# Optimization experiments

Measured on AMD Instinct MI355X. Metric: run time of the kernel, lower is better.

The kernel has to match this reference:

```python
import jax, jax.numpy as jnp
import numpy as np

HIDDEN = 4096
INTER = 11008
BATCH, SEQ = 2, 2048


def setup_inputs() -> dict:
    key = jax.random.key(0)
    ks = jax.random.split(key, 7)
    s_h = 1.0 / np.sqrt(HIDDEN)   # nn.Linear default init bound fan_in=HIDDEN
    s_i = 1.0 / np.sqrt(INTER)    # fan_in=INTER for down_proj
    return {
        "hidden_states": jax.random.normal(ks[0], (BATCH, SEQ, HIDDEN), dtype=jnp.float32),
        "w_gate": jax.random.uniform(ks[1], (INTER, HIDDEN), jnp.float32, -s_h, s_h),
        "b_gate": jax.random.uniform(ks[2], (INTER,), jnp.float32, -s_h, s_h),
        "w_up": jax.random.uniform(ks[3], (INTER, HIDDEN), jnp.float32, -s_h, s_h),
        "b_up": jax.random.uniform(ks[4], (INTER,), jnp.float32, -s_h, s_h),
        "w_down": jax.random.uniform(ks[5], (HIDDEN, INTER), jnp.float32, -s_i, s_i),
        "b_down": jax.random.uniform(ks[6], (HIDDEN,), jnp.float32, -s_i, s_i),
    }


def reference(hidden_states, w_gate, b_gate, w_up, b_up, w_down, b_down):
    # SwiGLU MLP: down( silu(gate(x)) * up(x) )
    gate = jax.nn.silu(jnp.einsum("bsh,ih->bsi", hidden_states, w_gate) + b_gate)
    up = jnp.einsum("bsh,ih->bsi", hidden_states, w_up) + b_up
    return jnp.einsum("bsi,hi->bsh", gate * up, w_down) + b_down
```

## Files before the change

kernel.cpp:

```cpp
#include <hip/hip_runtime.h>
#include <hip/hip_bf16.h>


#define M_TOK 4096
#define HID   4096
#define INT_  11008
#define NGU   1376
#define NCVT  160

typedef __attribute__((ext_vector_type(8))) short bf16x8;
typedef __attribute__((ext_vector_type(4))) float f32x4;

__device__ __forceinline__ unsigned short f2bf(float f) {
    union { float f; unsigned int u; } a; a.f = f;
    unsigned int u = a.u;
    u += 0x7fff + ((u >> 16) & 1);
    return (unsigned short)(u >> 16);
}

__global__ void cvt3(const float* __restrict__ x,  unsigned short* __restrict__ xb,
                     const float* __restrict__ wg, unsigned short* __restrict__ s1,
                     const float* __restrict__ wu, unsigned short* __restrict__ s2,
                     int n4x, int n4w) {
    const int total = n4x + 2 * n4w;
    const int stride = gridDim.x * blockDim.x;
    for (int i = blockIdx.x * blockDim.x + threadIdx.x; i < total; i += stride) {
        const float* src; unsigned short* dst; int j;
        if (i < n4x)            { j = i;             src = x;  dst = xb; }
        else if (i < n4x + n4w) { j = i - n4x;       src = wg; dst = s1; }
        else                    { j = i - n4x - n4w; src = wu; dst = s2; }
        float4 v = ((const float4*)src)[j];
        ushort4 o;
        o.x = f2bf(v.x); o.y = f2bf(v.y); o.z = f2bf(v.z); o.w = f2bf(v.w);
        ((ushort4*)dst)[j] = o;
    }
}

__global__ void cvt_f32_bf16(const float* __restrict__ in, unsigned short* __restrict__ out, int n4) {
    int stride = gridDim.x * blockDim.x;
    for (int i = blockIdx.x * blockDim.x + threadIdx.x; i < n4; i += stride) {
        float4 v = ((const float4*)in)[i];
        ushort4 o;
        o.x = f2bf(v.x); o.y = f2bf(v.y); o.z = f2bf(v.z); o.w = f2bf(v.w);
        ((ushort4*)out)[i] = o;
    }
}

#define GLL(gsrc, ldst) \
    __builtin_amdgcn_global_load_lds( \
        (__attribute__((address_space(1))) void*)(gsrc), \
        (__attribute__((address_space(3))) void*)(ldst), 16, 0, 0)

#define VMC(n) asm volatile("s_waitcnt vmcnt(" #n ")" ::: "memory")
#define BARR __builtin_amdgcn_s_barrier()
#define PIN  __builtin_amdgcn_sched_barrier(0)

__global__ __launch_bounds__(512, 2)
void gemm_gu(const unsigned short* __restrict__ A,
             const unsigned short* __restrict__ Wg,
             const unsigned short* __restrict__ Wu,
             const float* __restrict__ bg,
             const float* __restrict__ bu,
             unsigned short* __restrict__ T,
             const float* __restrict__ wdSrc,
             unsigned short* __restrict__ wdDst,
             int M, int NI, int K) {
    __shared__ unsigned short lds[2 * 32768];

    const int tid  = threadIdx.x;

    if (blockIdx.x >= NGU) {
        const int c = blockIdx.x - NGU;
        const int n4w = (INT_ * HID) / 4;
        const float4* src = (const float4*)wdSrc;
        ushort4* dst = (ushort4*)wdDst;
        for (int u = c * 512 + tid; u < n4w; u += NCVT * 512) {
            float4 v = src[u];
            ushort4 o;
            o.x = f2bf(v.x); o.y = f2bf(v.y); o.z = f2bf(v.z); o.w = f2bf(v.w);
            dst[u] = o;
        }
        return;
    }

    const int lane = tid & 63;
    const int w    = tid >> 6;
    const int wm   = w >> 2;
    const int wn   = w & 3;

    const int ntn = NI >> 7;
    const int chunk = NGU >> 3;
    const int sw = (blockIdx.x & 7) * chunk + (blockIdx.x >> 3);
    const int bm = sw / ntn, bn = sw % ntn;

    const unsigned short* Ag  = A  + (size_t)(bm * 256) * K;
    const unsigned short* Bgg = Wg + (size_t)(bn * 128) * K;
    const unsigned short* Bug = Wu + (size_t)(bn * 128) * K;

    int offA[2][2], offBW[2];
#pragma unroll
    for (int i = 0; i < 2; ++i) {
        int sig = i * 512 + tid;
        int r   = sig >> 3;
        int s   = (sig & 7) ^ (r & 7);
#pragma unroll
        for (int h = 0; h < 2; ++h) {
            int grow = ((r >> 6) * 2 + h) * 64 + (r & 63);
            offA[h][i] = grow * K + s * 8;
        }
        offBW[i] = r * K + s * 8;
    }

    const int rl = lane & 15;
    const int kg = lane >> 4;
    const int x  = rl & 7;
    const int aRow  = (wm * 64 + rl) * 64;
    const int bGoff = 16384 + (wn * 32 + rl) * 64;
    const int bUoff = 24576 + (wn * 32 + rl) * 64;
    int slt[2];
#pragma unroll
    for (int ks = 0; ks < 2; ++ks) slt[ks] = ((ks * 4 + kg) ^ x) * 8;

    f32x4 accg[2][8], accu[2][8];
#pragma unroll
    for (int q = 0; q < 2; ++q)
#pragma unroll
        for (int f = 0; f < 8; ++f) {
            accg[q][f] = (f32x4){0.f, 0.f, 0.f, 0.f};
            accu[q][f] = (f32x4){0.f, 0.f, 0.f, 0.f};
        }

    const int NT = K >> 6;

#define STAGE_A(H, DST, SRC) \
    GLL((SRC) + offA[H][0], (DST) + (H) * 8192 + tid * 8); \
    GLL((SRC) + offA[H][1], (DST) + (H) * 8192 + 4096 + tid * 8)
#define STAGE_W(BASE, DST, SRC) \
    GLL((SRC) + offBW[0], (DST) + (BASE) + tid * 8); \
    GLL((SRC) + offBW[1], (DST) + (BASE) + 4096 + tid * 8)

#define RD_A(BUF, QM, DST) \
    { _Pragma("unroll") for (int ks = 0; ks < 2; ++ks) \
      _Pragma("unroll") for (int fm = 0; fm < 4; ++fm) \
        DST[ks * 4 + fm] = *(const bf16x8*)((BUF) + (QM) * 8192 + aRow + fm * 1024 + slt[ks]); }
#define RD_W(BUF, ROFF, DST) \
    { _Pragma("unroll") for (int ks = 0; ks < 2; ++ks) \
      _Pragma("unroll") for (int fn = 0; fn < 2; ++fn) \
        DST[ks * 2 + fn] = *(const bf16x8*)((BUF) + (ROFF) + fn * 1024 + slt[ks]); }
#define Q16(ACC, QM, AF, BF) \
    { _Pragma("unroll") for (int ks = 0; ks < 2; ++ks) \
      _Pragma("unroll") for (int fm = 0; fm < 4; ++fm) \
      _Pragma("unroll") for (int fn = 0; fn < 2; ++fn) \
        ACC[QM][fm * 2 + fn] = __builtin_amdgcn_mfma_f32_16x16x32_bf16( \
            AF[ks * 4 + fm], BF[ks * 2 + fn], ACC[QM][fm * 2 + fn], 0, 0, 0); }

    bf16x8 A0f[8], A1f[8], Bgf[4], Buf_[4];

    STAGE_A(0, lds, Ag);
    STAGE_W(16384, lds, Bgg);
    STAGE_W(24576, lds, Bug);
    STAGE_A(1, lds, Ag);
    VMC(2);
    BARR; PIN;

    for (int t = 0; t < NT; ++t) {
        const unsigned short* bc = lds + (t & 1) * 32768;
        unsigned short* sb = lds + ((t + 1) & 1) * 32768;
        const int ts = (t + 1 < NT) ? (t + 1) : (NT - 1);
        const unsigned short* sA = Ag + (size_t)ts * 64;
        const unsigned short* sG = Bgg + (size_t)ts * 64;
        const unsigned short* sU = Bug + (size_t)ts * 64;

        RD_A(bc, 0, A0f);
        RD_W(bc, bGoff, Bgf);
        STAGE_A(0, sb, sA);
        Q16(accg, 0, A0f, Bgf);
        RD_W(bc, bUoff, Buf_);
        STAGE_W(16384, sb, sG);
        Q16(accu, 0, A0f, Buf_);
        STAGE_W(24576, sb, sU);
        VMC(6);
        BARR; PIN;

        RD_A(bc, 1, A1f);
        STAGE_A(1, sb, sA);
        Q16(accg, 1, A1f, Bgf);
        Q16(accu, 1, A1f, Buf_);
        VMC(2);
        BARR; PIN;
    }
#undef RD_A
#undef RD_W
#undef Q16
#undef STAGE_A
#undef STAGE_W

    const int rbase = bm * 256 + wm * 128 + (lane >> 4) * 4;
    const int cbase = bn * 128 + wn * 32 + (lane & 15);
#pragma unroll
    for (int qm = 0; qm < 2; ++qm)
#pragma unroll
        for (int fn = 0; fn < 2; ++fn) {
            const int col = cbase + fn * 16;
            const float bgv = bg[col];
            const float buv = bu[col];
#pragma unroll
            for (int fm = 0; fm < 4; ++fm) {
                const int rb = rbase + qm * 64 + fm * 16;
#pragma unroll
                for (int j = 0; j < 4; ++j) {
                    float g = accg[qm][fm * 2 + fn][j] + bgv;
                    float u = accu[qm][fm * 2 + fn][j] + buv;
                    float s = g / (1.f + __expf(-g)) * u;
                    T[(size_t)(rb + j) * (size_t)INT_ + col] = f2bf(s);
                }
            }
        }
}

__global__ __launch_bounds__(512, 2)
void gemm_dn(const unsigned short* __restrict__ A,
             const unsigned short* __restrict__ B,
             const float* __restrict__ bias,
             float* __restrict__ C,
             int M, int N, int K) {
    __shared__ unsigned short lds[2 * 32768];

    const int tid  = threadIdx.x;
    const int lane = tid & 63;
    const int w    = tid >> 6;
    const int wm   = w >> 2;
    const int wn   = w & 3;

    const int ntn = N >> 8;
    const int chunk = gridDim.x >> 3;
    const int sw = (blockIdx.x & 7) * chunk + (blockIdx.x >> 3);
    const int bm = sw / ntn, bn = sw % ntn;

    const unsigned short* Ag = A + (size_t)(bm * 256) * K;
    const unsigned short* Bg = B + (size_t)(bn * 256) * K;

    int offA[2][2], offB[2][2];
#pragma unroll
    for (int h = 0; h < 2; ++h)
#pragma unroll
        for (int i = 0; i < 2; ++i) {
            int sig = i * 512 + tid;
            int r   = sig >> 3;
            int s   = (sig & 7) ^ (r & 7);
            int grow = ((r >> 6) * 2 + h) * 64 + (r & 63);
            int gcol = ((r >> 5) * 2 + h) * 32 + (r & 31);
            offA[h][i] = grow * K + s * 8;
            offB[h][i] = gcol * K + s * 8;
        }

    const int rl = lane & 15;
    const int kg = lane >> 4;
    const int x  = rl & 7;
    const int aRow = (wm * 64 + rl) * 64;
    const int bRow = 16384 + (wn * 32 + rl) * 64;
    int slt[2];
#pragma unroll
    for (int ks = 0; ks < 2; ++ks) slt[ks] = ((ks * 4 + kg) ^ x) * 8;

    f32x4 acc[2][2][8];
#pragma unroll
    for (int qm = 0; qm < 2; ++qm)
#pragma unroll
        for (int qn = 0; qn < 2; ++qn)
#pragma unroll
            for (int f = 0; f < 8; ++f)
                acc[qm][qn][f] = (f32x4){0.f, 0.f, 0.f, 0.f};

    const int NT = K >> 6;

#define STAGE_A(H, DST, SRC) \
    GLL((SRC) + offA[H][0], (DST) + (H) * 8192 + tid * 8); \
    GLL((SRC) + offA[H][1], (DST) + (H) * 8192 + 4096 + tid * 8)
#define STAGE_B(H, DST, SRC) \
    GLL((SRC) + offB[H][0], (DST) + 16384 + (H) * 8192 + tid * 8); \
    GLL((SRC) + offB[H][1], (DST) + 16384 + (H) * 8192 + 4096 + tid * 8)
#define RD_A(BUF, QM, DST) \
    { _Pragma("unroll") for (int ks = 0; ks < 2; ++ks) \
      _Pragma("unroll") for (int fm = 0; fm < 4; ++fm) \
        DST[ks * 4 + fm] = *(const bf16x8*)((BUF) + (QM) * 8192 + aRow + fm * 1024 + slt[ks]); }
#define RD_B(BUF, QN, DST) \
    { _Pragma("unroll") for (int ks = 0; ks < 2; ++ks) \
      _Pragma("unroll") for (int fn = 0; fn < 2; ++fn) \
        DST[ks * 2 + fn] = *(const bf16x8*)((BUF) + (QN) * 8192 + bRow + fn * 1024 + slt[ks]); }
#define Q16(QM, QN, AF, BF) \
    { _Pragma("unroll") for (int ks = 0; ks < 2; ++ks) \
      _Pragma("unroll") for (int fm = 0; fm < 4; ++fm) \
      _Pragma("unroll") for (int fn = 0; fn < 2; ++fn) \
        acc[QM][QN][fm * 2 + fn] = __builtin_amdgcn_mfma_f32_16x16x32_bf16( \
            AF[ks * 4 + fm], BF[ks * 2 + fn], acc[QM][QN][fm * 2 + fn], 0, 0, 0); }

    bf16x8 A0f[8], A1f[8], B0f[4], B1f[4];

    STAGE_A(0, lds, Ag); STAGE_B(0, lds, Bg); STAGE_B(1, lds, Bg); STAGE_A(1, lds, Ag);
    VMC(2);
    BARR; PIN;

    for (int t = 0; t < NT; ++t) {
        const unsigned short* bc = lds + (t & 1) * 32768;
        unsigned short* sb = lds + ((t + 1) & 1) * 32768;
        const int ts = (t + 1 < NT) ? (t + 1) : (NT - 1);
        const unsigned short* sAt = Ag + (size_t)ts * 64;
        const unsigned short* sBt = Bg + (size_t)ts * 64;

        RD_A(bc, 0, A0f);
        RD_B(bc, 0, B0f);
        STAGE_A(0, sb, sAt);
        Q16(0, 0, A0f, B0f);
        RD_B(bc, 1, B1f);
        STAGE_B(0, sb, sBt);
        Q16(0, 1, A0f, B1f);
        STAGE_B(1, sb, sBt);
        VMC(6);
        BARR; PIN;

        RD_A(bc, 1, A1f);
        STAGE_A(1, sb, sAt);
        Q16(1, 1, A1f, B1f);
        Q16(1, 0, A1f, B0f);
        VMC(2);
        BARR; PIN;
    }
#undef RD_A
#undef RD_B
#undef Q16
#undef STAGE_A
#undef STAGE_B

    const int rbase = bm * 256 + wm * 128 + (lane >> 4) * 4;
    const int cbase = bn * 256 + wn * 64 + (lane & 15);
#pragma unroll
    for (int qm = 0; qm < 2; ++qm)
#pragma unroll
        for (int qn = 0; qn < 2; ++qn)
#pragma unroll
            for (int fn = 0; fn < 2; ++fn) {
                const int col = cbase + qn * 32 + fn * 16;
                const float bv = bias[col];
#pragma unroll
                for (int fm = 0; fm < 4; ++fm) {
                    const int rb = rbase + qm * 64 + fm * 16;
#pragma unroll
                    for (int j = 0; j < 4; ++j)
                        C[(size_t)(rb + j) * (size_t)N + col] = acc[qm][qn][fm * 2 + fn][j] + bv;
                }
            }
}

extern "C" void kernel_launch(void* const* d_in, const int* in_sizes, int n_in,
                              void* d_out, int out_size, void* d_ws, size_t ws_size,
                              hipStream_t stream) {
    const float* x  = (const float*)d_in[0];
    const float* wg = (const float*)d_in[1];
    const float* bg = (const float*)d_in[2];
    const float* wu = (const float*)d_in[3];
    const float* bu = (const float*)d_in[4];
    const float* wd = (const float*)d_in[5];
    const float* bd = (const float*)d_in[6];

    const size_t NX = (size_t)M_TOK * HID;
    const size_t NW = (size_t)INT_ * HID;

    unsigned short* ws = (unsigned short*)d_ws;
    unsigned short* Xb = ws;
    unsigned short* S1 = Xb + NX;
    unsigned short* S2 = S1 + NW;
    unsigned short* S3 = S2 + NW;
    unsigned short* S4 = S3 + NW;

    const bool fused = ws_size >= (NX + 4 * NW) * 2;

    dim3 blk512(512);
    dim3 blk256(256);

    cvt3<<<2048, blk256, 0, stream>>>(x, Xb, wg, S1, wu, S2,
                                      (int)(NX / 4), (int)(NW / 4));

    if (fused) {
        gemm_gu<<<dim3(NGU + NCVT), blk512, 0, stream>>>(Xb, S1, S2, bg, bu, S3,
                                                         wd, S4, M_TOK, INT_, HID);
        gemm_dn<<<dim3(16 * 16), blk512, 0, stream>>>(S3, S4, bd, (float*)d_out,
                                                      M_TOK, HID, INT_);
    } else {
        gemm_gu<<<dim3(NGU), blk512, 0, stream>>>(Xb, S1, S2, bg, bu, S3,
                                                  (const float*)nullptr,
                                                  (unsigned short*)nullptr,
                                                  M_TOK, INT_, HID);
        cvt_f32_bf16<<<2048, blk256, 0, stream>>>(wd, S1, (int)(NW / 4));
        gemm_dn<<<dim3(16 * 16), blk512, 0, stream>>>(S3, S1, bd, (float*)d_out,
                                                      M_TOK, HID, INT_);
    }
}
```

Baseline: 993.7 us.

## Load B fragments directly from global into register double-buffers, bypassing LDS

```diff
diff --git a/kernel.cpp b/kernel.cpp
--- a/kernel.cpp
+++ b/kernel.cpp
@@ -65,7 +65,7 @@
              const float* __restrict__ wdSrc,
              unsigned short* __restrict__ wdDst,
              int M, int NI, int K) {
-    __shared__ unsigned short lds[2 * 32768];
+    __shared__ unsigned short lds[2 * 16384];
 
     const int tid  = threadIdx.x;
 
@@ -97,7 +97,7 @@
     const unsigned short* Bgg = Wg + (size_t)(bn * 128) * K;
     const unsigned short* Bug = Wu + (size_t)(bn * 128) * K;
 
-    int offA[2][2], offBW[2];
+    int offA[2][2];
 #pragma unroll
     for (int i = 0; i < 2; ++i) {
         int sig = i * 512 + tid;
@@ -108,18 +108,18 @@
             int grow = ((r >> 6) * 2 + h) * 64 + (r & 63);
             offA[h][i] = grow * K + s * 8;
         }
-        offBW[i] = r * K + s * 8;
     }
 
     const int rl = lane & 15;
     const int kg = lane >> 4;
     const int x  = rl & 7;
-    const int aRow  = (wm * 64 + rl) * 64;
-    const int bGoff = 16384 + (wn * 32 + rl) * 64;
-    const int bUoff = 24576 + (wn * 32 + rl) * 64;
+    const int aRow = (wm * 64 + rl) * 64;
     int slt[2];
 #pragma unroll
     for (int ks = 0; ks < 2; ++ks) slt[ks] = ((ks * 4 + kg) ^ x) * 8;
+
+    const unsigned short* BgL = Bgg + (size_t)(wn * 32 + rl) * K + kg * 8;
+    const unsigned short* BuL = Bug + (size_t)(wn * 32 + rl) * K + kg * 8;
 
     f32x4 accg[2][8], accu[2][8];
 #pragma unroll
@@ -135,18 +135,14 @@
 #define STAGE_A(H, DST, SRC) \
     GLL((SRC) + offA[H][0], (DST) + (H) * 8192 + tid * 8); \
     GLL((SRC) + offA[H][1], (DST) + (H) * 8192 + 4096 + tid * 8)
-#define STAGE_W(BASE, DST, SRC) \
-    GLL((SRC) + offBW[0], (DST) + (BASE) + tid * 8); \
-    GLL((SRC) + offBW[1], (DST) + (BASE) + 4096 + tid * 8)
-
 #define RD_A(BUF, QM, DST) \
     { _Pragma("unroll") for (int ks = 0; ks < 2; ++ks) \
       _Pragma("unroll") for (int fm = 0; fm < 4; ++fm) \
         DST[ks * 4 + fm] = *(const bf16x8*)((BUF) + (QM) * 8192 + aRow + fm * 1024 + slt[ks]); }
-#define RD_W(BUF, ROFF, DST) \
+#define LOADB(BASE, TS, DST) \
     { _Pragma("unroll") for (int ks = 0; ks < 2; ++ks) \
       _Pragma("unroll") for (int fn = 0; fn < 2; ++fn) \
-        DST[ks * 2 + fn] = *(const bf16x8*)((BUF) + (ROFF) + fn * 1024 + slt[ks]); }
+        DST[ks * 2 + fn] = *(const bf16x8*)((BASE) + (size_t)fn * 16 * K + (size_t)(TS) * 64 + ks * 32); }
 #define Q16(ACC, QM, AF, BF) \
     { _Pragma("unroll") for (int ks = 0; ks < 2; ++ks) \
       _Pragma("unroll") for (int fm = 0; fm < 4; ++fm) \
@@ -154,46 +150,47 @@
         ACC[QM][fm * 2 + fn] = __builtin_amdgcn_mfma_f32_16x16x32_bf16( \
             AF[ks * 4 + fm], BF[ks * 2 + fn], ACC[QM][fm * 2 + fn], 0, 0, 0); }
 
-    bf16x8 A0f[8], A1f[8], Bgf[4], Buf_[4];
+    bf16x8 A0f[8], A1f[8], BgA[4], BuA[4], BgB[4], BuB[4];
 
     STAGE_A(0, lds, Ag);
-    STAGE_W(16384, lds, Bgg);
-    STAGE_W(24576, lds, Bug);
     STAGE_A(1, lds, Ag);
-    VMC(2);
+    PIN;
+    LOADB(BgL, 0, BgA);
+    LOADB(BuL, 0, BuA);
+    VMC(8);
     BARR; PIN;
 
-    for (int t = 0; t < NT; ++t) {
-        const unsigned short* bc = lds + (t & 1) * 32768;
-        unsigned short* sb = lds + ((t + 1) & 1) * 32768;
-        const int ts = (t + 1 < NT) ? (t + 1) : (NT - 1);
-        const unsigned short* sA = Ag + (size_t)ts * 64;
-        const unsigned short* sG = Bgg + (size_t)ts * 64;
-        const unsigned short* sU = Bug + (size_t)ts * 64;
-
-        RD_A(bc, 0, A0f);
-        RD_W(bc, bGoff, Bgf);
-        STAGE_A(0, sb, sA);
-        Q16(accg, 0, A0f, Bgf);
-        RD_W(bc, bUoff, Buf_);
-        STAGE_W(16384, sb, sG);
-        Q16(accu, 0, A0f, Buf_);
-        STAGE_W(24576, sb, sU);
-        VMC(6);
-        BARR; PIN;
-
-        RD_A(bc, 1, A1f);
-        STAGE_A(1, sb, sA);
-        Q16(accg, 1, A1f, Bgf);
-        Q16(accu, 1, A1f, Buf_);
-        VMC(2);
-        BARR; PIN;
-    }
+#define TILE_GU(T, BGC, BUC, BGN, BUN)                                          \
+    {                                                                           \
+        const unsigned short* bc = lds + ((T) & 1) * 16384;                     \
+        unsigned short* sb = lds + (((T) + 1) & 1) * 16384;                     \
+        const int ts = ((T) + 1 < NT) ? ((T) + 1) : (NT - 1);                   \
+        const unsigned short* sA = Ag + (size_t)ts * 64;                        \
+        RD_A(bc, 0, A0f);                                                       \
+        STAGE_A(0, sb, sA);                                                     \
+        STAGE_A(1, sb, sA);                                                     \
+        PIN;                                                                    \
+        LOADB(BgL, ts, BGN);                                                    \
+        LOADB(BuL, ts, BUN);                                                    \
+        Q16(accg, 0, A0f, BGC);                                                 \
+        Q16(accu, 0, A0f, BUC);                                                 \
+        BARR; PIN;                                                              \
+        RD_A(bc, 1, A1f);                                                       \
+        Q16(accg, 1, A1f, BGC);                                                 \
+        Q16(accu, 1, A1f, BUC);                                                 \
+        VMC(8);                           \
+        BARR; PIN;                                                              \
+    }
+
+    for (int t = 0; t < NT; t += 2) {
+        TILE_GU(t,     BgA, BuA, BgB, BuB);
+        TILE_GU(t + 1, BgB, BuB, BgA, BuA);
+    }
+#undef TILE_GU
 #undef RD_A
-#undef RD_W
+#undef LOADB
 #undef Q16
 #undef STAGE_A
-#undef STAGE_W
 
     const int rbase = bm * 256 + wm * 128 + (lane >> 4) * 4;
     const int cbase = bn * 128 + wn * 32 + (lane & 15);
@@ -224,7 +221,7 @@
              const float* __restrict__ bias,
              float* __restrict__ C,
              int M, int N, int K) {
-    __shared__ unsigned short lds[2 * 32768];
+    __shared__ unsigned short lds[2 * 16384];
 
     const int tid  = threadIdx.x;
     const int lane = tid & 63;
@@ -240,28 +237,28 @@
     const unsigned short* Ag = A + (size_t)(bm * 256) * K;
     const unsigned short* Bg = B + (size_t)(bn * 256) * K;
 
-    int offA[2][2], offB[2][2];
-#pragma unroll
-    for (int h = 0; h < 2; ++h)
-#pragma unroll
-        for (int i = 0; i < 2; ++i) {
-            int sig = i * 512 + tid;
-            int r   = sig >> 3;
-            int s   = (sig & 7) ^ (r & 7);
+    int offA[2][2];
+#pragma unroll
+    for (int i = 0; i < 2; ++i) {
+        int sig = i * 512 + tid;
+        int r   = sig >> 3;
+        int s   = (sig & 7) ^ (r & 7);
+#pragma unroll
+        for (int h = 0; h < 2; ++h) {
             int grow = ((r >> 6) * 2 + h) * 64 + (r & 63);
-            int gcol = ((r >> 5) * 2 + h) * 32 + (r & 31);
             offA[h][i] = grow * K + s * 8;
-            offB[h][i] = gcol * K + s * 8;
-        }
+        }
+    }
 
     const int rl = lane & 15;
     const int kg = lane >> 4;
     const int x  = rl & 7;
     const int aRow = (wm * 64 + rl) * 64;
-    const int bRow = 16384 + (wn * 32 + rl) * 64;
     int slt[2];
 #pragma unroll
     for (int ks = 0; ks < 2; ++ks) slt[ks] = ((ks * 4 + kg) ^ x) * 8;
+
+    const unsigned short* BL = Bg + (size_t)(wn * 64 + rl) * K + kg * 8;
 
     f32x4 acc[2][2][8];
 #pragma unroll
@@ -277,17 +274,15 @@
 #define STAGE_A(H, DST, SRC) \
     GLL((SRC) + offA[H][0], (DST) + (H) * 8192 + tid * 8); \
     GLL((SRC) + offA[H][1], (DST) + (H) * 8192 + 4096 + tid * 8)
-#define STAGE_B(H, DST, SRC) \
-    GLL((SRC) + offB[H][0], (DST) + 16384 + (H) * 8192 + tid * 8); \
-    GLL((SRC) + offB[H][1], (DST) + 16384 + (H) * 8192 + 4096 + tid * 8)
 #define RD_A(BUF, QM, DST) \
     { _Pragma("unroll") for (int ks = 0; ks < 2; ++ks) \
       _Pragma("unroll") for (int fm = 0; fm < 4; ++fm) \
         DST[ks * 4 + fm] = *(const bf16x8*)((BUF) + (QM) * 8192 + aRow + fm * 1024 + slt[ks]); }
-#define RD_B(BUF, QN, DST) \
-    { _Pragma("unroll") for (int ks = 0; ks < 2; ++ks) \
-      _Pragma("unroll") for (int fn = 0; fn < 2; ++fn) \
-        DST[ks * 2 + fn] = *(const bf16x8*)((BUF) + (QN) * 8192 + bRow + fn * 1024 + slt[ks]); }
+#define LOADB_DN(TS, D0, D1) \
+    { _Pragma("unroll") for (int ks = 0; ks < 2; ++ks) \
+      _Pragma("unroll") for (int fn = 0; fn < 2; ++fn) { \
+        D0[ks * 2 + fn] = *(const bf16x8*)(BL + (size_t)(fn * 16) * K + (size_t)(TS) * 64 + ks * 32); \
+        D1[ks * 2 + fn] = *(const bf16x8*)(BL + (size_t)(32 + fn * 16) * K + (size_t)(TS) * 64 + ks * 32); } }
 #define Q16(QM, QN, AF, BF) \
     { _Pragma("unroll") for (int ks = 0; ks < 2; ++ks) \
       _Pragma("unroll") for (int fm = 0; fm < 4; ++fm) \
@@ -295,42 +290,45 @@
         acc[QM][QN][fm * 2 + fn] = __builtin_amdgcn_mfma_f32_16x16x32_bf16( \
             AF[ks * 4 + fm], BF[ks * 2 + fn], acc[QM][QN][fm * 2 + fn], 0, 0, 0); }
 
-    bf16x8 A0f[8], A1f[8], B0f[4], B1f[4];
-
-    STAGE_A(0, lds, Ag); STAGE_B(0, lds, Bg); STAGE_B(1, lds, Bg); STAGE_A(1, lds, Ag);
-    VMC(2);
+    bf16x8 A0f[8], A1f[8], B0A[4], B1A[4], B0B[4], B1B[4];
+
+    STAGE_A(0, lds, Ag);
+    STAGE_A(1, lds, Ag);
+    PIN;
+    LOADB_DN(0, B0A, B1A);
+    VMC(8);
     BARR; PIN;
 
-    for (int t = 0; t < NT; ++t) {
-        const unsigned short* bc = lds + (t & 1) * 32768;
-        unsigned short* sb = lds + ((t + 1) & 1) * 32768;
-        const int ts = (t + 1 < NT) ? (t + 1) : (NT - 1);
-        const unsigned short* sAt = Ag + (size_t)ts * 64;
-        const unsigned short* sBt = Bg + (size_t)ts * 64;
-
-        RD_A(bc, 0, A0f);
-        RD_B(bc, 0, B0f);
-        STAGE_A(0, sb, sAt);
-        Q16(0, 0, A0f, B0f);
-        RD_B(bc, 1, B1f);
-        STAGE_B(0, sb, sBt);
-        Q16(0, 1, A0f, B1f);
-        STAGE_B(1, sb, sBt);
-        VMC(6);
-        BARR; PIN;
-
-        RD_A(bc, 1, A1f);
-        STAGE_A(1, sb, sAt);
-        Q16(1, 1, A1f, B1f);
-        Q16(1, 0, A1f, B0f);
-        VMC(2);
-        BARR; PIN;
-    }
+#define TILE_DN(T, B0C, B1C, B0N, B1N)                                          \
+    {                                                                           \
+        const unsigned short* bc = lds + ((T) & 1) * 16384;                     \
+        unsigned short* sb = lds + (((T) + 1) & 1) * 16384;                     \
+        const int ts = ((T) + 1 < NT) ? ((T) + 1) : (NT - 1);                   \
+        const unsigned short* sA = Ag + (size_t)ts * 64;                        \
+        RD_A(bc, 0, A0f);                                                       \
+        STAGE_A(0, sb, sA);                                                     \
+        STAGE_A(1, sb, sA);                                                     \
+        PIN;                                                                    \
+        LOADB_DN(ts, B0N, B1N);                                                 \
+        Q16(0, 0, A0f, B0C);                                                    \
+        Q16(0, 1, A0f, B1C);                                                    \
+        BARR; PIN;                                                              \
+        RD_A(bc, 1, A1f);                                                       \
+        Q16(1, 1, A1f, B1C);                                                    \
+        Q16(1, 0, A1f, B0C);                                                    \
+        VMC(8);                                                                 \
+        BARR; PIN;                                                              \
+    }
+
+    for (int t = 0; t < NT; t += 2) {
+        TILE_DN(t,     B0A, B1A, B0B, B1B);
+        TILE_DN(t + 1, B0B, B1B, B0A, B1A);
+    }
+#undef TILE_DN
 #undef RD_A
-#undef RD_B
+#undef LOADB_DN
 #undef Q16
 #undef STAGE_A
-#undef STAGE_B
 
     const int rbase = bm * 256 + wm * 128 + (lane >> 4) * 4;
     const int cbase = bn * 256 + wn * 64 + (lane & 15);
```

Measured after the change: 1.514 ms. 52.3% more time.
